# Kernel optimization log

Hardware: AMD Instinct MI355X
Metric: run time of the kernel (lower is better)

## Reference

```python
import jax, jax.numpy as jnp
import numpy as np

B, C, N, H = 4, 256, 4096, 4
DK = C // H


def _proj(x, w, b):
    # Conv1d with kernel size 1 == per-point linear: [B,C,N] x [O,C] -> [B,O,N]
    return jnp.einsum('oc,bcn->bon', w, x) + b[None, :, None]


def setup_inputs() -> dict:
    key = jax.random.key(0)
    ks = jax.random.split(key, 9)
    s = 1.0 / np.sqrt(C)
    return {
        'x': jax.random.normal(ks[0], (B, C, N), jnp.float32),
        'wq': jax.random.normal(ks[1], (C, C), jnp.float32) * s,
        'bq': jax.random.normal(ks[2], (C,), jnp.float32) * 0.01,
        'wk': jax.random.normal(ks[3], (C, C), jnp.float32) * s,
        'bk': jax.random.normal(ks[4], (C,), jnp.float32) * 0.01,
        'wv': jax.random.normal(ks[5], (C, C), jnp.float32) * s,
        'bv': jax.random.normal(ks[6], (C,), jnp.float32) * 0.01,
        'wp': jax.random.normal(ks[7], (C, C), jnp.float32) * s,
        'bp': jax.random.normal(ks[8], (C,), jnp.float32) * 0.01,
    }


def reference(x, wq, bq, wk, bk, wv, bv, wp, bp):
    b, c, n = x.shape
    q = _proj(x, wq, bq).reshape(b, H, DK, n)
    k = _proj(x, wk, bk).reshape(b, H, DK, n)
    v = _proj(x, wv, bv).reshape(b, H, DK, n)
    scale = 1.0 / jnp.sqrt(jnp.asarray(DK, x.dtype))
    # scores over point pairs: [B,H,N,N]
    scores = jnp.einsum('bhdn,bhdm->bhnm', q, k) * scale
    attn = jax.nn.softmax(scores, axis=-1)
    out = jnp.einsum('bhnm,bhdm->bhdn', attn, v)  # [B,H,DK,N]
    out = out.reshape(b, c, n)
    out = _proj(out, wp, bp)
    return out + x
```

## Files before the change

### kernel.cpp

```cpp
#include <hip/hip_runtime.h>


#define BDIM 4
#define CDIM 256
#define NDIM 4096
#define HDIM 4
#define DKDIM 64
#define NQ   (BDIM * HDIM * NDIM)
#define NSPLIT 2
#define KPERZ (NDIM / NSPLIT)
#define QSCALE 0.18033688011112042f
#define WSZ (CDIM * CDIM)

typedef __bf16 bf16x8 __attribute__((ext_vector_type(8)));
typedef float f32x4 __attribute__((ext_vector_type(4)));
typedef short s16x4 __attribute__((ext_vector_type(4)));
typedef unsigned short u16;
typedef unsigned int u32;

__device__ __forceinline__ u16 f2bf(float f) {
  union { __bf16 h; u16 s; } u; u.h = (__bf16)f; return u.s;
}
__device__ __forceinline__ float bf2f(u16 v) {
  union { u32 u; float f; } x; x.u = (u32)v << 16; return x.f;
}
__device__ __forceinline__ u32 pk2(float a, float b) {
  return (u32)f2bf(a) | ((u32)f2bf(b) << 16);
}
__device__ __forceinline__ void gload16(const u16* g, u16* l) {
  __builtin_amdgcn_global_load_lds(
      (const __attribute__((address_space(1))) void*)g,
      (__attribute__((address_space(3))) void*)l, 16, 0, 0);
}

__global__ __launch_bounds__(256) void wconv_kernel(
    const float* __restrict__ wq, const float* __restrict__ wk,
    const float* __restrict__ wv, const float* __restrict__ wp,
    u16* __restrict__ wb)
{
  const int a = blockIdx.y;
  const float* src = (a == 0) ? wq : (a == 1) ? wk : (a == 2) ? wv : wp;
  const float sc = (a == 0) ? QSCALE : 1.0f;
  const int i = (blockIdx.x * 256 + threadIdx.x) * 8;
  const float4 v0 = *(const float4*)(src + i);
  const float4 v1 = *(const float4*)(src + i + 4);
  union { u32 p[4]; uint4 q; } o;
  o.p[0] = pk2(v0.x * sc, v0.y * sc);
  o.p[1] = pk2(v0.z * sc, v0.w * sc);
  o.p[2] = pk2(v1.x * sc, v1.y * sc);
  o.p[3] = pk2(v1.z * sc, v1.w * sc);
  *(uint4*)(wb + (size_t)a * WSZ + i) = o.q;
}

__global__ __launch_bounds__(256) void xt_kernel(
    const float* __restrict__ x, u16* __restrict__ xT)
{
  const int b = blockIdx.z, c0 = blockIdx.y * 64, n0 = blockIdx.x * 64;
  __shared__ __align__(16) float T[64][68];
  const int t = threadIdx.x;
  {
    const int cr = t >> 4, nc = (t & 15) * 4;
    #pragma unroll
    for (int ci = 0; ci < 4; ++ci) {
      const float4 v = *(const float4*)&x[((size_t)(b * CDIM + c0 + cr + ci * 16)) * NDIM + n0 + nc];
      *(float4*)&T[cr + ci * 16][nc] = v;
    }
  }
  __syncthreads();
  {
    const int n = t >> 2, g = t & 3;
    union { u16 u[16]; uint4 v[2]; } pk;
    #pragma unroll
    for (int u_ = 0; u_ < 16; ++u_) pk.u[u_] = f2bf(T[g * 16 + u_][n]);
    uint4* dst = (uint4*)&xT[((size_t)(b * NDIM + n0 + n)) * CDIM + c0 + g * 16];
    dst[0] = pk.v[0]; dst[1] = pk.v[1];
  }
}

__global__ __launch_bounds__(256, 4) void qkv_kernel(
    const u16* __restrict__ xT, const u16* __restrict__ wb,
    const float* __restrict__ bq, const float* __restrict__ bk,
    const float* __restrict__ bv,
    u16* __restrict__ qT, u16* __restrict__ kT, u16* __restrict__ vB)
{
  const int b = blockIdx.z;
  const int p = blockIdx.y >> 1;
  const int o0 = (blockIdx.y & 1) * 128;
  const int n0 = blockIdx.x * 64;
  const float* bsel = (p == 0) ? bq : (p == 1) ? bk : bv;
  const float wscale = (p == 0) ? QSCALE : 1.0f;

  __shared__ __align__(16) u16 XTs[64][264];
  const int t = threadIdx.x, lane = t & 63, w = t >> 6;
  const int qd = lane >> 4, lm = lane & 15;
  const int sr = t >> 2, sg = (t & 3) * 8;

  {
    const u16* xsrc = xT + ((size_t)(b * NDIM + n0 + sr)) * CDIM + sg;
    #pragma unroll
    for (int cs = 0; cs < 8; ++cs)
      *(uint4*)&XTs[sr][cs * 32 + sg] = *(const uint4*)(xsrc + cs * 32);
  }
  __syncthreads();

  const u16* wrow0 = wb + (size_t)p * WSZ + (size_t)(o0 + 32 * w + lm) * CDIM + qd * 8;
  const u16* wrow1 = wrow0 + (size_t)16 * CDIM;

  f32x4 acc[4][2];
  #pragma unroll
  for (int nt = 0; nt < 4; ++nt)
    #pragma unroll
    for (int j = 0; j < 2; ++j) acc[nt][j] = (f32x4){0.f, 0.f, 0.f, 0.f};

  #pragma unroll
  for (int cs = 0; cs < 8; ++cs) {
    const bf16x8 wf0 = *(const bf16x8*)(wrow0 + cs * 32);
    const bf16x8 wf1 = *(const bf16x8*)(wrow1 + cs * 32);
    bf16x8 xf[4];
    #pragma unroll
    for (int nt = 0; nt < 4; ++nt)
      xf[nt] = *(const bf16x8*)&XTs[16 * nt + lm][cs * 32 + qd * 8];
    #pragma unroll
    for (int nt = 0; nt < 4; ++nt) {
      if (p < 2) {
        acc[nt][0] = __builtin_amdgcn_mfma_f32_16x16x32_bf16(xf[nt], wf0, acc[nt][0], 0, 0, 0);
        acc[nt][1] = __builtin_amdgcn_mfma_f32_16x16x32_bf16(xf[nt], wf1, acc[nt][1], 0, 0, 0);
      } else {
        acc[nt][0] = __builtin_amdgcn_mfma_f32_16x16x32_bf16(wf0, xf[nt], acc[nt][0], 0, 0, 0);
        acc[nt][1] = __builtin_amdgcn_mfma_f32_16x16x32_bf16(wf1, xf[nt], acc[nt][1], 0, 0, 0);
      }
    }
  }

  if (p < 2) {
    u16* out = (p == 0) ? qT : kT;
    #pragma unroll
    for (int j = 0; j < 2; ++j) {
      const int og = o0 + 32 * w + 16 * j + lm;
      const float bv2 = bsel[og] * wscale;
      #pragma unroll
      for (int nt = 0; nt < 4; ++nt)
        #pragma unroll
        for (int r = 0; r < 4; ++r) {
          const int n = n0 + 16 * nt + 4 * qd + r;
          out[((size_t)(b * NDIM + n)) * CDIM + og] = f2bf(acc[nt][j][r] + bv2);
        }
    }
  } else {
    #pragma unroll
    for (int j = 0; j < 2; ++j) {
      const float4 b4 = *(const float4*)&bsel[o0 + 32 * w + 16 * j + 4 * qd];
      const float bvr[4] = {b4.x, b4.y, b4.z, b4.w};
      #pragma unroll
      for (int nt = 0; nt < 4; ++nt)
        #pragma unroll
        for (int r = 0; r < 4; ++r) {
          const int og = o0 + 32 * w + 16 * j + 4 * qd + r;
          const int n = n0 + 16 * nt + lm;
          vB[((size_t)(b * CDIM + og)) * NDIM + n] = f2bf(acc[nt][j][r] + bvr[r]);
        }
    }
  }
}

__global__ __launch_bounds__(256, 4) void attn_kernel(
    const u16* __restrict__ qT, const u16* __restrict__ kT,
    const u16* __restrict__ vB, u16* __restrict__ Opart,
    float* __restrict__ Lp)
{
  const int bh = blockIdx.y, b = bh >> 2, h = bh & 3;
  const int n0 = blockIdx.x * 128;
  const int z  = blockIdx.z;

  __shared__ __align__(16) u16 KVlds[2][2][64][64];

  const int t = threadIdx.x, lane = t & 63, w = t >> 6;
  const int qd = lane >> 4, lm = lane & 15, l7 = lm & 7;

  bf16x8 qf[2][2];
  {
    const u16* qbase = qT + ((size_t)(b * NDIM) + n0) * CDIM + h * 64;
    #pragma unroll
    for (int s = 0; s < 2; ++s)
      #pragma unroll
      for (int hh = 0; hh < 2; ++hh)
        qf[s][hh] = *(const bf16x8*)(qbase +
            (size_t)(16 * (2 * w + s) + lm) * CDIM + 32 * hh + qd * 8);
  }

  const s16x4 ones = (s16x4){(short)0x3F80, (short)0x3F80, (short)0x3F80, (short)0x3F80};
  f32x4 la[2];
  la[0] = (f32x4){0.f, 0.f, 0.f, 0.f};
  la[1] = (f32x4){0.f, 0.f, 0.f, 0.f};

  f32x4 oa[2][4];
  #pragma unroll
  for (int s = 0; s < 2; ++s)
    #pragma unroll
    for (int dt = 0; dt < 4; ++dt) oa[s][dt] = (f32x4){0.f, 0.f, 0.f, 0.f};

  const int srow = lane >> 3;
  const int swz  = 8 * ((lane & 7) ^ srow);
  const u16* kp0 = kT + ((size_t)(b * NDIM + z * KPERZ + 8 * w + srow)) * CDIM + h * 64 + swz;
  const u16* kp1 = kp0 + (size_t)32 * CDIM;
  const u16* vp0 = vB + ((size_t)(b * CDIM + h * 64 + 8 * w + srow)) * NDIM + z * KPERZ + swz;
  const u16* vp1 = vp0 + (size_t)32 * NDIM;

  {
    u16* kb = &KVlds[0][0][0][0];
    u16* vb2 = &KVlds[0][1][0][0];
    gload16(kp0, kb + w * 512);
    gload16(kp1, kb + (4 + w) * 512);
    gload16(vp0, vb2 + w * 512);
    gload16(vp1, vb2 + (4 + w) * 512);
  }

  #pragma unroll 1
  for (int it = 0; it < KPERZ / 64; ++it) {
    __syncthreads();
    if (it + 1 < KPERZ / 64) {
      const size_t ko = (size_t)(it + 1) * 64 * CDIM;
      const int    vo = (it + 1) * 64;
      u16* kb = &KVlds[(it + 1) & 1][0][0][0];
      u16* vb2 = &KVlds[(it + 1) & 1][1][0][0];
      gload16(kp0 + ko, kb + w * 512);
      gload16(kp1 + ko, kb + (4 + w) * 512);
      gload16(vp0 + vo, vb2 + w * 512);
      gload16(vp1 + vo, vb2 + (4 + w) * 512);
    }
    const u16 (*Kt)[64] = KVlds[it & 1][0];
    const u16 (*Vt)[64] = KVlds[it & 1][1];

    union { u16 u[4]; u32 d[2]; s16x4 v; } pk[2][4];

    #pragma unroll
    for (int nt = 0; nt < 4; ++nt) {
      const bf16x8 kf0 = *(const bf16x8*)&Kt[16 * nt + lm][8 * (qd ^ l7)];
      const bf16x8 kf1 = *(const bf16x8*)&Kt[16 * nt + lm][8 * ((4 + qd) ^ l7)];
      #pragma unroll
      for (int s = 0; s < 2; ++s) {
        f32x4 zz = (f32x4){0.f, 0.f, 0.f, 0.f};
        zz = __builtin_amdgcn_mfma_f32_16x16x32_bf16(kf0, qf[s][0], zz, 0, 0, 0);
        zz = __builtin_amdgcn_mfma_f32_16x16x32_bf16(kf1, qf[s][1], zz, 0, 0, 0);
        const float p0 = __builtin_amdgcn_exp2f(zz[0]);
        const float p1 = __builtin_amdgcn_exp2f(zz[1]);
        const float p2 = __builtin_amdgcn_exp2f(zz[2]);
        const float p3 = __builtin_amdgcn_exp2f(zz[3]);
        pk[s][nt].d[0] = pk2(p0, p1);
        pk[s][nt].d[1] = pk2(p2, p3);
      }
    }

    #pragma unroll
    for (int c = 0; c < 4; ++c) {
      s16x4 av[4];
      #pragma unroll
      for (int dt = 0; dt < 4; ++dt)
        av[dt] = *(const s16x4*)&Vt[16 * dt + lm][(16 * c + 4 * qd) ^ (8 * l7)];
      la[0] = __builtin_amdgcn_mfma_f32_16x16x16bf16_1k(ones, pk[0][c].v, la[0], 0, 0, 0);
      la[1] = __builtin_amdgcn_mfma_f32_16x16x16bf16_1k(ones, pk[1][c].v, la[1], 0, 0, 0);
      #pragma unroll
      for (int dt = 0; dt < 4; ++dt) {
        oa[0][dt] = __builtin_amdgcn_mfma_f32_16x16x16bf16_1k(av[dt], pk[0][c].v, oa[0][dt], 0, 0, 0);
        oa[1][dt] = __builtin_amdgcn_mfma_f32_16x16x16bf16_1k(av[dt], pk[1][c].v, oa[1][dt], 0, 0, 0);
      }
    }
  }

  const float l_i[2] = {la[0][0], la[1][0]};

  __syncthreads();
  u16 (*Ot)[72] = (u16(*)[72])&KVlds[0][0][0][0];
  #pragma unroll
  for (int s = 0; s < 2; ++s) {
    const float inv = 1.0f / l_i[s];
    #pragma unroll
    for (int dt = 0; dt < 4; ++dt)
      #pragma unroll
      for (int r = 0; r < 4; ++r)
        Ot[16 * (2 * w + s) + lm][16 * dt + 4 * qd + r] = f2bf(oa[s][dt][r] * inv);
  }
  if (qd == 0) {
    const size_t lbase = ((size_t)z * (BDIM * HDIM) + bh) * NDIM;
    #pragma unroll
    for (int s = 0; s < 2; ++s)
      Lp[lbase + n0 + 16 * (2 * w + s) + lm] = l_i[s];
  }
  __syncthreads();
  {
    const int r = t >> 1, g = (t & 1) * 32;
    u16* dst = Opart + (((size_t)z * (BDIM * HDIM) + bh) * NDIM + n0 + r) * DKDIM + g;
    const uint4* srcp = (const uint4*)&Ot[r][g];
    uint4* d4 = (uint4*)dst;
    d4[0] = srcp[0]; d4[1] = srcp[1]; d4[2] = srcp[2]; d4[3] = srcp[3];
  }
}

__global__ __launch_bounds__(256, 4) void projout_kernel(
    const u16* __restrict__ Opart, const float* __restrict__ Lp,
    const u16* __restrict__ wb, const float* __restrict__ bp,
    const float* __restrict__ res, float* __restrict__ out)
{
  const int b = blockIdx.z, o0 = blockIdx.y * 128, n0 = blockIdx.x * 64;
  __shared__ __align__(16) u16 XTs[64][40];
  const int t = threadIdx.x, lane = t & 63, w = t >> 6;
  const int qd = lane >> 4, lm = lane & 15;
  const int sr = t >> 2, sg = (t & 3) * 8;

  float wh[4][NSPLIT];
  #pragma unroll
  for (int hh = 0; hh < 4; ++hh) {
    const size_t i0 = ((size_t)(b * HDIM + hh)) * NDIM + n0 + sr;
    float l[NSPLIT], tot = 0.f;
    #pragma unroll
    for (int zz = 0; zz < NSPLIT; ++zz) { l[zz] = Lp[(size_t)zz * NQ + i0]; tot += l[zz]; }
    const float iv = 1.0f / tot;
    #pragma unroll
    for (int zz = 0; zz < NSPLIT; ++zz) wh[hh][zz] = l[zz] * iv;
  }

  const u16* wrow0 = wb + (size_t)3 * WSZ + (size_t)(o0 + 32 * w + lm) * CDIM + qd * 8;
  const u16* wrow1 = wrow0 + (size_t)16 * CDIM;

  f32x4 acc[4][2];
  #pragma unroll
  for (int nt = 0; nt < 4; ++nt)
    #pragma unroll
    for (int j = 0; j < 2; ++j) acc[nt][j] = (f32x4){0.f, 0.f, 0.f, 0.f};

  for (int cs = 0; cs < 8; ++cs) {
    const int c0 = cs * 32;
    const int hh = c0 >> 6;
    const int dk = (c0 & 63) + sg;
    const bf16x8 wf0 = *(const bf16x8*)(wrow0 + c0);
    const bf16x8 wf1 = *(const bf16x8*)(wrow1 + c0);
    __syncthreads();
    {
      const size_t obase = (((size_t)(b * HDIM + hh)) * NDIM + n0 + sr) * DKDIM + dk;
      float v[8] = {0.f, 0.f, 0.f, 0.f, 0.f, 0.f, 0.f, 0.f};
      #pragma unroll
      for (int zz = 0; zz < NSPLIT; ++zz) {
        union { u16 u[8]; uint4 q; } a;
        a.q = *(const uint4*)(Opart + (size_t)zz * NQ * DKDIM + obase);
        const float wz = wh[hh][zz];
        #pragma unroll
        for (int j = 0; j < 8; ++j) v[j] = fmaf(wz, bf2f(a.u[j]), v[j]);
      }
      union { u16 u[8]; uint4 q; } ov;
      #pragma unroll
      for (int j = 0; j < 8; ++j) ov.u[j] = f2bf(v[j]);
      *(uint4*)&XTs[sr][sg] = ov.q;
    }
    __syncthreads();
    bf16x8 xf[4];
    #pragma unroll
    for (int nt = 0; nt < 4; ++nt) xf[nt] = *(const bf16x8*)&XTs[16 * nt + lm][qd * 8];
    #pragma unroll
    for (int nt = 0; nt < 4; ++nt) {
      acc[nt][0] = __builtin_amdgcn_mfma_f32_16x16x32_bf16(wf0, xf[nt], acc[nt][0], 0, 0, 0);
      acc[nt][1] = __builtin_amdgcn_mfma_f32_16x16x32_bf16(wf1, xf[nt], acc[nt][1], 0, 0, 0);
    }
  }

  #pragma unroll
  for (int j = 0; j < 2; ++j) {
    const float4 b4 = *(const float4*)&bp[o0 + 32 * w + 16 * j + 4 * qd];
    const float bvr[4] = {b4.x, b4.y, b4.z, b4.w};
    #pragma unroll
    for (int nt = 0; nt < 4; ++nt)
      #pragma unroll
      for (int r = 0; r < 4; ++r) {
        const int og = o0 + 32 * w + 16 * j + 4 * qd + r;
        const int n = n0 + 16 * nt + lm;
        const size_t idx = ((size_t)(b * CDIM + og)) * NDIM + n;
        out[idx] = acc[nt][j][r] + bvr[r] + res[idx];
      }
  }
}

extern "C" void kernel_launch(void* const* d_in, const int* in_sizes, int n_in,
                              void* d_out, int out_size, void* d_ws, size_t ws_size,
                              hipStream_t stream)
{
  const float* x  = (const float*)d_in[0];
  const float* wq = (const float*)d_in[1];
  const float* bq = (const float*)d_in[2];
  const float* wk = (const float*)d_in[3];
  const float* bk = (const float*)d_in[4];
  const float* wv = (const float*)d_in[5];
  const float* bv = (const float*)d_in[6];
  const float* wp = (const float*)d_in[7];
  const float* bp = (const float*)d_in[8];
  float* out = (float*)d_out;

  const size_t sz = (size_t)BDIM * CDIM * NDIM;
  u16* xTb = (u16*)d_ws;
  u16* qTb = xTb + sz;
  u16* kTb = qTb + sz;
  u16* vBb = kTb + sz;
  u16* Opart = vBb + sz;
  float* Lp = (float*)(Opart + (size_t)NSPLIT * sz);
  u16* wbf = (u16*)(Lp + (size_t)NSPLIT * NQ);

  const dim3 blk(256);
  wconv_kernel<<<dim3(WSZ / (256 * 8), 4, 1), blk, 0, stream>>>(wq, wk, wv, wp, wbf);
  xt_kernel<<<dim3(NDIM / 64, CDIM / 64, BDIM), blk, 0, stream>>>(x, xTb);
  qkv_kernel<<<dim3(NDIM / 64, 6, BDIM), blk, 0, stream>>>(
      xTb, wbf, bq, bk, bv, qTb, kTb, vBb);
  attn_kernel<<<dim3(NDIM / 128, BDIM * HDIM, NSPLIT), blk, 0, stream>>>(
      qTb, kTb, vBb, Opart, Lp);
  projout_kernel<<<dim3(NDIM / 64, 2, BDIM), blk, 0, stream>>>(
      Opart, Lp, wbf, bp, x, out);
}
```

Baseline: 198.9 us.

## Widen attention blocks to 512 threads covering 256 queries per K/V tile

```diff
diff --git a/kernel.cpp b/kernel.cpp
--- a/kernel.cpp
+++ b/kernel.cpp
@@ -163,13 +163,13 @@
   }
 }
 
-__global__ __launch_bounds__(256, 4) void attn_kernel(
+__global__ __launch_bounds__(512, 4) void attn_kernel(
     const u16* __restrict__ qT, const u16* __restrict__ kT,
     const u16* __restrict__ vB, u16* __restrict__ Opart,
     float* __restrict__ Lp)
 {
   const int bh = blockIdx.y, b = bh >> 2, h = bh & 3;
-  const int n0 = blockIdx.x * 128;
+  const int n0 = blockIdx.x * 256;
   const int z  = blockIdx.z;
 
   __shared__ __align__(16) u16 KVlds[2][2][64][64];
@@ -202,18 +202,10 @@
   const int srow = lane >> 3;
   const int swz  = 8 * ((lane & 7) ^ srow);
   const u16* kp0 = kT + ((size_t)(b * NDIM + z * KPERZ + 8 * w + srow)) * CDIM + h * 64 + swz;
-  const u16* kp1 = kp0 + (size_t)32 * CDIM;
   const u16* vp0 = vB + ((size_t)(b * CDIM + h * 64 + 8 * w + srow)) * NDIM + z * KPERZ + swz;
-  const u16* vp1 = vp0 + (size_t)32 * NDIM;
-
-  {
-    u16* kb = &KVlds[0][0][0][0];
-    u16* vb2 = &KVlds[0][1][0][0];
-    gload16(kp0, kb + w * 512);
-    gload16(kp1, kb + (4 + w) * 512);
-    gload16(vp0, vb2 + w * 512);
-    gload16(vp1, vb2 + (4 + w) * 512);
-  }
+
+  gload16(kp0, &KVlds[0][0][0][0] + w * 512);
+  gload16(vp0, &KVlds[0][1][0][0] + w * 512);
 
   #pragma unroll 1
   for (int it = 0; it < KPERZ / 64; ++it) {
@@ -221,12 +213,8 @@
     if (it + 1 < KPERZ / 64) {
       const size_t ko = (size_t)(it + 1) * 64 * CDIM;
       const int    vo = (it + 1) * 64;
-      u16* kb = &KVlds[(it + 1) & 1][0][0][0];
-      u16* vb2 = &KVlds[(it + 1) & 1][1][0][0];
-      gload16(kp0 + ko, kb + w * 512);
-      gload16(kp1 + ko, kb + (4 + w) * 512);
-      gload16(vp0 + vo, vb2 + w * 512);
-      gload16(vp1 + vo, vb2 + (4 + w) * 512);
+      gload16(kp0 + ko, &KVlds[(it + 1) & 1][0][0][0] + w * 512);
+      gload16(vp0 + vo, &KVlds[(it + 1) & 1][1][0][0] + w * 512);
     }
     const u16 (*Kt)[64] = KVlds[it & 1][0];
     const u16 (*Vt)[64] = KVlds[it & 1][1];
@@ -269,30 +257,38 @@
 
   const float l_i[2] = {la[0][0], la[1][0]};
 
+  if (qd == 0) {
+    const size_t lbase = ((size_t)z * (BDIM * HDIM) + bh) * NDIM;
+    #pragma unroll
+    for (int s = 0; s < 2; ++s)
+      Lp[lbase + n0 + 16 * (2 * w + s) + lm] = l_i[s];
+  }
+
   __syncthreads();
   u16 (*Ot)[72] = (u16(*)[72])&KVlds[0][0][0][0];
   #pragma unroll
-  for (int s = 0; s < 2; ++s) {
-    const float inv = 1.0f / l_i[s];
-    #pragma unroll
-    for (int dt = 0; dt < 4; ++dt)
-      #pragma unroll
-      for (int r = 0; r < 4; ++r)
-        Ot[16 * (2 * w + s) + lm][16 * dt + 4 * qd + r] = f2bf(oa[s][dt][r] * inv);
-  }
-  if (qd == 0) {
-    const size_t lbase = ((size_t)z * (BDIM * HDIM) + bh) * NDIM;
-    #pragma unroll
-    for (int s = 0; s < 2; ++s)
-      Lp[lbase + n0 + 16 * (2 * w + s) + lm] = l_i[s];
-  }
-  __syncthreads();
-  {
-    const int r = t >> 1, g = (t & 1) * 32;
-    u16* dst = Opart + (((size_t)z * (BDIM * HDIM) + bh) * NDIM + n0 + r) * DKDIM + g;
-    const uint4* srcp = (const uint4*)&Ot[r][g];
-    uint4* d4 = (uint4*)dst;
-    d4[0] = srcp[0]; d4[1] = srcp[1]; d4[2] = srcp[2]; d4[3] = srcp[3];
+  for (int ph = 0; ph < 2; ++ph) {
+    if ((w >> 2) == ph) {
+      const int wl = w & 3;
+      #pragma unroll
+      for (int s = 0; s < 2; ++s) {
+        const float inv = 1.0f / l_i[s];
+        #pragma unroll
+        for (int dt = 0; dt < 4; ++dt)
+          #pragma unroll
+          for (int r = 0; r < 4; ++r)
+            Ot[16 * (2 * wl + s) + lm][16 * dt + 4 * qd + r] = f2bf(oa[s][dt][r] * inv);
+      }
+    }
+    __syncthreads();
+    {
+      const int r = t >> 2, g = (t & 3) * 16;
+      u16* dst = Opart + (((size_t)z * (BDIM * HDIM) + bh) * NDIM + n0 + ph * 128 + r) * DKDIM + g;
+      const uint4* srcp = (const uint4*)&Ot[r][g];
+      uint4* d4 = (uint4*)dst;
+      d4[0] = srcp[0]; d4[1] = srcp[1];
+    }
+    __syncthreads();
   }
 }
 
@@ -407,7 +403,7 @@
   xt_kernel<<<dim3(NDIM / 64, CDIM / 64, BDIM), blk, 0, stream>>>(x, xTb);
   qkv_kernel<<<dim3(NDIM / 64, 6, BDIM), blk, 0, stream>>>(
       xTb, wbf, bq, bk, bv, qTb, kTb, vBb);
-  attn_kernel<<<dim3(NDIM / 128, BDIM * HDIM, NSPLIT), blk, 0, stream>>>(
+  attn_kernel<<<dim3(NDIM / 256, BDIM * HDIM, NSPLIT), dim3(512), 0, stream>>>(
       qTb, kTb, vBb, Opart, Lp);
   projout_kernel<<<dim3(NDIM / 64, 2, BDIM), blk, 0, stream>>>(
       Opart, Lp, wbf, bp, x, out);
```

After: 195.9 us. Within noise of the previous version (-1.5%).
